# Kernel optimization log

Measured on AMD Instinct MI355X. Metric: run time of the kernel, lower is better.

Reference implementation:

```python
import jax, jax.numpy as jnp
import numpy as np

N, D, R, E = 20000, 256, 12, 200000  # nodes, feat dim, relation labels, edges


def setup_inputs() -> dict:
    key = jax.random.key(0)
    ks = jax.random.split(key, 8)
    x = jax.random.normal(ks[0], (N, D), dtype=jnp.float32)
    dep_idx = jax.random.randint(ks[1], (E,), 0, N)
    rel_idx = jax.random.randint(ks[2], (E,), 0, R)
    gov_idx = jax.random.randint(ks[3], (E,), 0, N)
    # nn.Linear params: W is [out,in], y = x @ W.T + b
    W_self = jax.random.normal(ks[4], (D, D), dtype=jnp.float32) * 0.02
    b_self = jnp.zeros((D,), dtype=jnp.float32)
    # 2R relation weights: [0..R) forward labels, [R..2R) reversed '_r' labels
    W_rel = jax.random.normal(ks[5], (2 * R, D, D), dtype=jnp.float32) * 0.02
    b_rel = jax.random.normal(ks[6], (2 * R, D), dtype=jnp.float32) * 0.02
    return {"x": x, "dep_idx": dep_idx, "rel_idx": rel_idx, "gov_idx": gov_idx,
            "W_self": W_self, "b_self": b_self, "W_rel": W_rel, "b_rel": b_rel}


def reference(x, dep_idx, rel_idx, gov_idx, W_self, b_self, W_rel, b_rel):
    R_ = W_rel.shape[0] // 2
    # self transform for every node
    out = x @ W_self.T + b_self  # [N, D]
    # all-relation transform, grouped GEMM instead of per-edge Linear calls
    T = jnp.einsum('nd,rod->nro', x, W_rel)  # [N, 2R, D]
    # forward edges: dependent += W[rel] @ x[governor] + b[rel]
    msg_f = T[gov_idx, rel_idx] + b_rel[rel_idx]          # [E, D]
    # reverse edges: governor += W[rel_r] @ x[dependent] + b[rel_r]
    msg_r = T[dep_idx, rel_idx + R_] + b_rel[rel_idx + R_]  # [E, D]
    out = out.at[dep_idx].add(msg_f).at[gov_idx].add(msg_r)
    return jax.nn.relu(out)
```

## Files before the change

kernel.cpp:

```cpp
#include <hip/hip_runtime.h>
#include <cstdint>
#include <cstddef>

#define DD 256
#define NSLOT 25
#define SELFSLOT 12

typedef unsigned short u16;
typedef __bf16 bf16t;
typedef bf16t bf16x8 __attribute__((ext_vector_type(8)));
typedef unsigned short us8 __attribute__((ext_vector_type(8)));
typedef unsigned short us4 __attribute__((ext_vector_type(4)));
typedef float f32x4 __attribute__((ext_vector_type(4)));

__device__ __forceinline__ u16 f2bf(float f) {
    uint32_t u = __builtin_bit_cast(uint32_t, f);
    u += 0x7FFFu + ((u >> 16) & 1u);
    return (u16)(u >> 16);
}
__device__ __forceinline__ float bf2f(u16 h) {
    uint32_t u = ((uint32_t)h) << 16;
    return __builtin_bit_cast(float, u);
}

__global__ void k_convert(const float* __restrict__ s, u16* __restrict__ d, int n) {
    int i = blockIdx.x * blockDim.x + threadIdx.x;
    int st = gridDim.x * blockDim.x;
    for (; i < n; i += st) d[i] = f2bf(s[i]);
}

__global__ void k_bias(const float* __restrict__ b_self, const float* __restrict__ b_rel,
                       float* __restrict__ dst) {
    int i = blockIdx.x * 256 + threadIdx.x;
    if (i >= NSLOT * DD) return;
    int s = i >> 8, n = i & 255;
    float v;
    if (s < SELFSLOT) v = b_rel[s * DD + n];
    else if (s == SELFSLOT) v = b_self[n];
    else v = b_rel[(s - 1) * DD + n];
    dst[i] = v;
}

__global__ void k_zero(int* p, int n) {
    int i = blockIdx.x * blockDim.x + threadIdx.x;
    if (i < n) p[i] = 0;
}

__global__ void k_mark(const int* __restrict__ dep, const int* __restrict__ rel,
                       const int* __restrict__ gov, int E, int N, int* __restrict__ flag) {
    int i = blockIdx.x * blockDim.x + threadIdx.x;
    int st = gridDim.x * blockDim.x;
    for (int j = i; j < E; j += st) {
        int r = rel[j];
        flag[r * N + gov[j]] = 1;
        flag[(13 + r) * N + dep[j]] = 1;
    }
    for (int j = i; j < N; j += st) flag[SELFSLOT * N + j] = 1;
}

__global__ void k_scan1(const int* __restrict__ counts, int* __restrict__ csr,
                        int* __restrict__ bsum, int B2) {
    __shared__ int sm[256];
    int tid = threadIdx.x;
    int i = blockIdx.x * 256 + tid;
    int v = (i < B2) ? counts[i] : 0;
    sm[tid] = v;
    __syncthreads();
    for (int off = 1; off < 256; off <<= 1) {
        int t = (tid >= off) ? sm[tid - off] : 0;
        __syncthreads();
        sm[tid] += t;
        __syncthreads();
    }
    if (i < B2) csr[i] = sm[tid] - v;
    if (tid == 255) bsum[blockIdx.x] = sm[255];
}

__global__ void k_scan2(const int* __restrict__ bsum, int* __restrict__ bbase, int nb) {
    __shared__ int sm[256];
    int t = threadIdx.x;
    int pre[8];
    int tot = 0;
    for (int j = 0; j < 8; ++j) {
        int idx = t * 8 + j;
        int v = (idx < nb) ? bsum[idx] : 0;
        pre[j] = tot;
        tot += v;
    }
    sm[t] = tot;
    __syncthreads();
    for (int off = 1; off < 256; off <<= 1) {
        int x = (t >= off) ? sm[t - off] : 0;
        __syncthreads();
        sm[t] += x;
        __syncthreads();
    }
    int base = sm[t] - tot;
    for (int j = 0; j < 8; ++j) {
        int idx = t * 8 + j;
        if (idx < nb) bbase[idx] = base + pre[j];
    }
}

__global__ void k_scan3f(int* __restrict__ pos, const int* __restrict__ bbase,
                         const int* __restrict__ flag, int B2) {
    int i = blockIdx.x * 256 + threadIdx.x;
    if (i < B2) {
        int v = pos[i] + bbase[i >> 8];
        pos[i] = v;
        if (i == B2 - 1) pos[B2] = v + flag[i];
    }
}

__global__ void k_scan3(int* __restrict__ csr, int* __restrict__ cursor,
                        const int* __restrict__ bbase, int B2, int E2) {
    int i = blockIdx.x * 256 + threadIdx.x;
    if (i < B2) {
        int v = csr[i] + bbase[i >> 8];
        csr[i] = v;
        cursor[i] = v;
    }
    if (i == 0) csr[B2] = E2;
}

__global__ void k_rk(const int* __restrict__ flag, const int* __restrict__ pos,
                     int* __restrict__ rksrc, int NN, int N) {
    int i = blockIdx.x * 256 + threadIdx.x;
    if (i >= NN) return;
    if (flag[i]) {
        int slot = i / N;
        rksrc[pos[i]] = i - slot * N;
    }
}

__global__ void k_hist(const int* __restrict__ dep, const int* __restrict__ rel,
                       const int* __restrict__ gov, int E, int N, int SG,
                       int* __restrict__ cnt) {
    int i = blockIdx.x * blockDim.x + threadIdx.x;
    int st = gridDim.x * blockDim.x;
    for (; i < E; i += st) {
        int r = rel[i];
        atomicAdd(&cnt[(r / SG) * N + dep[i]], 1);
        atomicAdd(&cnt[((13 + r) / SG) * N + gov[i]], 1);
    }
}

__global__ void k_scatter(const int* __restrict__ dep, const int* __restrict__ rel,
                          const int* __restrict__ gov, int E, int N, int SG,
                          const int* __restrict__ pos,
                          int* __restrict__ cursor, int* __restrict__ epay) {
    int i = blockIdx.x * blockDim.x + threadIdx.x;
    int st = gridDim.x * blockDim.x;
    for (; i < E; i += st) {
        int r = rel[i], d = dep[i], g = gov[i];
        int g0 = r / SG;
        int p = atomicAdd(&cursor[g0 * N + d], 1);
        epay[p] = pos[r * N + g] - pos[g0 * SG * N];
        int gs = 13 + r;
        int g1 = gs / SG;
        int q = atomicAdd(&cursor[g1 * N + g], 1);
        epay[q] = pos[gs * N + d] - pos[g1 * SG * N];
    }
}

__global__ __launch_bounds__(256) void k_T(
    const u16* __restrict__ xb, const u16* __restrict__ Wb, const float* __restrict__ ba,
    const int* __restrict__ pos, const int* __restrict__ rksrc, u16* __restrict__ T,
    int N, int gslot0, int tilesPerSlot) {
    __shared__ u16 sm[2 * 128 * 72];
    __shared__ int s_src[128];
    u16 (*As)[72] = (u16(*)[72])sm;
    u16 (*Bs)[72] = (u16(*)[72])(sm + 128 * 72);

    const int bx = blockIdx.x;
    const int slot = bx / tilesPerSlot;
    const int mtile = bx - slot * tilesPerSlot;
    const int gslot = gslot0 + slot;
    const int u0 = pos[gslot * N];
    const int used = pos[(gslot + 1) * N] - u0;
    const int row0 = mtile * 128;
    if (row0 >= used) return;
    const int gbase = pos[gslot0 * N];
    const int n0 = blockIdx.y * 128;
    const int tid = threadIdx.x;

    if (tid < 128) {
        int r = row0 + tid;
        s_src[tid] = rksrc[u0 + ((r < used) ? r : (used - 1))];
    }
    __syncthreads();

    const int lane = tid & 63, wv = tid >> 6;
    const int wr = wv & 1, wc = wv >> 1;
    const int l15 = lane & 15, quad = lane >> 4;
    const int srow = tid >> 1, sh = (tid & 1) * 32;
    const u16* bgp = Wb + ((size_t)gslot << 16) + (size_t)(n0 + srow) * DD + sh;

    f32x4 acc[4][4] = {};
    for (int kb = 0; kb < DD; kb += 64) {
        {
            const us8* ga = (const us8*)(xb + (size_t)s_src[srow] * DD + kb + sh);
            us8 a0 = ga[0], a1 = ga[1], a2 = ga[2], a3 = ga[3];
            *(us8*)&As[srow][sh]      = a0;
            *(us8*)&As[srow][sh + 8]  = a1;
            *(us8*)&As[srow][sh + 16] = a2;
            *(us8*)&As[srow][sh + 24] = a3;
            const us8* gb = (const us8*)(bgp + kb);
            us8 b0 = gb[0], b1 = gb[1], b2 = gb[2], b3 = gb[3];
            *(us8*)&Bs[srow][sh]      = b0;
            *(us8*)&Bs[srow][sh + 8]  = b1;
            *(us8*)&Bs[srow][sh + 16] = b2;
            *(us8*)&Bs[srow][sh + 24] = b3;
        }
        __syncthreads();
        #pragma unroll
        for (int ks = 0; ks < 2; ++ks) {
            const int kk = ks * 32 + quad * 8;
            bf16x8 af[4], bfv[4];
            #pragma unroll
            for (int mt = 0; mt < 4; ++mt)
                af[mt] = __builtin_bit_cast(bf16x8, *(const us8*)&As[wr * 64 + mt * 16 + l15][kk]);
            #pragma unroll
            for (int nt = 0; nt < 4; ++nt)
                bfv[nt] = __builtin_bit_cast(bf16x8, *(const us8*)&Bs[wc * 64 + nt * 16 + l15][kk]);
            #pragma unroll
            for (int mt = 0; mt < 4; ++mt)
                #pragma unroll
                for (int nt = 0; nt < 4; ++nt)
                    acc[mt][nt] = __builtin_amdgcn_mfma_f32_16x16x32_bf16(
                        af[mt], bfv[nt], acc[mt][nt], 0, 0, 0);
        }
        __syncthreads();
    }

    float bv[4];
    #pragma unroll
    for (int nt = 0; nt < 4; ++nt) bv[nt] = ba[gslot * DD + n0 + wc * 64 + nt * 16 + l15];
    u16* trb = sm + wv * (64 * 72);
    #pragma unroll
    for (int nt = 0; nt < 4; ++nt)
        #pragma unroll
        for (int mt = 0; mt < 4; ++mt)
            #pragma unroll
            for (int j = 0; j < 4; ++j)
                trb[(mt * 16 + quad * 4 + j) * 72 + nt * 16 + l15] =
                    f2bf(acc[mt][nt][j] + bv[nt]);
    __syncthreads();
    const int trow0 = u0 - gbase + row0 + wr * 64;
    const int half = lane & 1;
    #pragma unroll
    for (int it = 0; it < 2; ++it) {
        int r = it * 32 + (lane >> 1);
        if (row0 + wr * 64 + r < used) {
            const us8* sp = (const us8*)(trb + r * 72 + half * 32);
            us8 v0 = sp[0], v1 = sp[1], v2 = sp[2], v3 = sp[3];
            us8* dp = (us8*)(T + (size_t)(trow0 + r) * DD + n0 + wc * 64 + half * 32);
            dp[0] = v0; dp[1] = v1; dp[2] = v2; dp[3] = v3;
        }
    }
}

__global__ __launch_bounds__(256) void k_gather(
    const u16* __restrict__ T, const int* __restrict__ epay,
    const int* __restrict__ csr, const int* __restrict__ pos,
    float* __restrict__ out, int N, int bktBase, int selfKeyBase, int gfN,
    int first, int last) {
    int wid = (blockIdx.x * 256 + threadIdx.x) >> 6;
    if (wid >= N) return;
    int feat = (threadIdx.x & 63) * 4;
    f32x4 a = {0.0f, 0.0f, 0.0f, 0.0f};
    if (!first) a = *(const f32x4*)(out + (size_t)wid * DD + feat);
    if (selfKeyBase >= 0) {
        int p = pos[selfKeyBase + wid] - pos[gfN];
        us4 v = *(const us4*)(T + (size_t)p * DD + feat);
        a[0] += bf2f(v[0]); a[1] += bf2f(v[1]); a[2] += bf2f(v[2]); a[3] += bf2f(v[3]);
    }
    int beg = csr[bktBase + wid], end = csr[bktBase + wid + 1];
    f32x4 b = {0.0f, 0.0f, 0.0f, 0.0f};
    int j = beg;
    for (; j + 1 < end; j += 2) {
        int p0 = epay[j], p1 = epay[j + 1];
        us4 v0 = *(const us4*)(T + (size_t)p0 * DD + feat);
        us4 v1 = *(const us4*)(T + (size_t)p1 * DD + feat);
        a[0] += bf2f(v0[0]); a[1] += bf2f(v0[1]); a[2] += bf2f(v0[2]); a[3] += bf2f(v0[3]);
        b[0] += bf2f(v1[0]); b[1] += bf2f(v1[1]); b[2] += bf2f(v1[2]); b[3] += bf2f(v1[3]);
    }
    if (j < end) {
        int p0 = epay[j];
        us4 v0 = *(const us4*)(T + (size_t)p0 * DD + feat);
        a[0] += bf2f(v0[0]); a[1] += bf2f(v0[1]); a[2] += bf2f(v0[2]); a[3] += bf2f(v0[3]);
    }
    a[0] += b[0]; a[1] += b[1]; a[2] += b[2]; a[3] += b[3];
    if (last) {
        a[0] = fmaxf(a[0], 0.0f); a[1] = fmaxf(a[1], 0.0f);
        a[2] = fmaxf(a[2], 0.0f); a[3] = fmaxf(a[3], 0.0f);
    }
    *(f32x4*)(out + (size_t)wid * DD + feat) = a;
}

extern "C" void kernel_launch(void* const* d_in, const int* in_sizes, int n_in,
                              void* d_out, int out_size, void* d_ws, size_t ws_size,
                              hipStream_t stream) {
    const float* x      = (const float*)d_in[0];
    const int*   dep    = (const int*)  d_in[1];
    const int*   rel    = (const int*)  d_in[2];
    const int*   gov    = (const int*)  d_in[3];
    const float* W_self = (const float*)d_in[4];
    const float* b_self = (const float*)d_in[5];
    const float* W_rel  = (const float*)d_in[6];
    const float* b_rel  = (const float*)d_in[7];
    float* out = (float*)d_out;

    const int N  = in_sizes[0] / DD;
    const int E  = in_sizes[1];
    const int NN = NSLOT * N;

    char* w = (char*)d_ws;
    auto alloc = [&](size_t bytes) {
        char* p = w;
        w += (bytes + 255) & ~(size_t)255;
        return p;
    };
    u16* xb    = (u16*)alloc((size_t)N * DD * sizeof(u16));
    u16* Wb    = (u16*)alloc((size_t)NSLOT * DD * DD * sizeof(u16));
    float* ba  = (float*)alloc((size_t)NSLOT * DD * sizeof(float));
    int* flag  = (int*)alloc((size_t)NN * sizeof(int));
    int* pos   = (int*)alloc(((size_t)NN + 1) * sizeof(int));
    int* rksrc = (int*)alloc(((size_t)2 * E + N) * sizeof(int));
    int* bcsr  = (int*)alloc(((size_t)6 * N + 1) * sizeof(int));
    int* bcur  = (int*)alloc((size_t)6 * N * sizeof(int));
    int* bsum  = (int*)alloc((size_t)2048 * sizeof(int));
    int* bbas  = (int*)alloc((size_t)2048 * sizeof(int));
    int* epay  = (int*)alloc((size_t)2 * E * sizeof(int));

    size_t used = (size_t)(w - (char*)d_ws);
    size_t avail = (ws_size > used) ? (ws_size - used) : 0;

    int NGROUP = 2, SG = 13;
    for (int ng = 1; ng <= 5; ++ng) {
        int sg = (NSLOT + ng - 1) / ng;
        size_t maxB = 0;
        for (int g = 0; g < ng; ++g) {
            int s0 = g * sg, s1 = s0 + sg; if (s1 > NSLOT) s1 = NSLOT;
            if (s0 >= NSLOT) break;
            int hasSelf = (s0 <= SELFSLOT && SELFSLOT < s1) ? 1 : 0;
            size_t rels = (size_t)(s1 - s0 - hasSelf);
            size_t rows = rels * N; if (rows > (size_t)2 * E) rows = (size_t)2 * E;
            rows += hasSelf ? (size_t)N : 0;
            if (rows > maxB) maxB = rows;
        }
        if (maxB * ((size_t)DD * 2) <= avail) { NGROUP = ng; SG = sg; break; }
        NGROUP = ng + 1; SG = (NSLOT + NGROUP - 1) / NGROUP;
    }
    u16* T = (u16*)w;

    k_convert<<<1024, 256, 0, stream>>>(x, xb, N * DD);
    k_convert<<<1024, 256, 0, stream>>>(W_rel, Wb, 12 * DD * DD);
    k_convert<<<64, 256, 0, stream>>>(W_self, Wb + (size_t)SELFSLOT * DD * DD, DD * DD);
    k_convert<<<1024, 256, 0, stream>>>(W_rel + (size_t)12 * DD * DD,
                                        Wb + (size_t)13 * DD * DD, 12 * DD * DD);
    k_bias<<<(NSLOT * DD + 255) / 256, 256, 0, stream>>>(b_self, b_rel, ba);

    const int fBlocks = (NN + 255) / 256;
    k_zero<<<fBlocks, 256, 0, stream>>>(flag, NN);
    k_mark<<<512, 256, 0, stream>>>(dep, rel, gov, E, N, flag);
    k_scan1<<<fBlocks, 256, 0, stream>>>(flag, pos, bsum, NN);
    k_scan2<<<1, 256, 0, stream>>>(bsum, bbas, fBlocks);
    k_scan3f<<<fBlocks, 256, 0, stream>>>(pos, bbas, flag, NN);
    k_rk<<<fBlocks, 256, 0, stream>>>(flag, pos, rksrc, NN, N);

    int* bcnt = flag;
    const int B2 = NGROUP * N;
    const int bBlocks = (B2 + 255) / 256;
    k_zero<<<bBlocks, 256, 0, stream>>>(bcnt, B2);
    k_hist<<<256, 256, 0, stream>>>(dep, rel, gov, E, N, SG, bcnt);
    k_scan1<<<bBlocks, 256, 0, stream>>>(bcnt, bcsr, bsum, B2);
    k_scan2<<<1, 256, 0, stream>>>(bsum, bbas, bBlocks);
    k_scan3<<<bBlocks, 256, 0, stream>>>(bcsr, bcur, bbas, B2, 2 * E);
    k_scatter<<<(E + 255) / 256, 256, 0, stream>>>(dep, rel, gov, E, N, SG, pos, bcur, epay);

    const int tilesPerSlot = (N + 127) / 128;
    const int gBlocks = (N + 3) / 4;
    for (int g = 0; g < NGROUP; ++g) {
        int s0 = g * SG;
        if (s0 >= NSLOT) break;
        int Sg = NSLOT - s0; if (Sg > SG) Sg = SG;
        k_T<<<dim3(Sg * tilesPerSlot, 2), 256, 0, stream>>>(
            xb, Wb, ba, pos, rksrc, T, N, s0, tilesPerSlot);
        int hasSelf = (s0 <= SELFSLOT && SELFSLOT < s0 + Sg);
        k_gather<<<gBlocks, 256, 0, stream>>>(
            T, epay, bcsr, pos, out, N, g * N,
            hasSelf ? SELFSLOT * N : -1, s0 * N,
            (g == 0) ? 1 : 0, (g == NGROUP - 1) ? 1 : 0);
    }
}
```

Baseline: 305.8 us.

## Fuse preprocessing kernels and unroll gather loop by four

Merges the five conversion/bias kernels into one, fuses flag marking with the bucket histogram, and runs the two prefix-scan pipelines together in shared scan kernels. The rank-source build and the CSR finalisation are folded into one third-pass kernel, and zeroing switches to memset. The goal is to cut roughly a dozen small launches and their serialization gaps. The gather loop is also unrolled to four independent accumulators for more memory-level parallelism, and the histogram now gets its own buffer instead of reusing flag.

```diff
diff --git a/kernel.cpp b/kernel.cpp
--- a/kernel.cpp
+++ b/kernel.cpp
@@ -23,47 +23,64 @@
     return __builtin_bit_cast(float, u);
 }
 
-__global__ void k_convert(const float* __restrict__ s, u16* __restrict__ d, int n) {
+__global__ void k_convert_all(const float* __restrict__ x, const float* __restrict__ W_rel,
+                              const float* __restrict__ W_self, const float* __restrict__ b_self,
+                              const float* __restrict__ b_rel,
+                              u16* __restrict__ xb, u16* __restrict__ Wb,
+                              float* __restrict__ ba, int NDD) {
+    const int s0 = NDD;
+    const int s1 = s0 + 12 * 65536;
+    const int s2 = s1 + 65536;
+    const int s3 = s2 + 12 * 65536;
+    const int s4 = s3 + NSLOT * DD;
     int i = blockIdx.x * blockDim.x + threadIdx.x;
     int st = gridDim.x * blockDim.x;
-    for (; i < n; i += st) d[i] = f2bf(s[i]);
-}
-
-__global__ void k_bias(const float* __restrict__ b_self, const float* __restrict__ b_rel,
-                       float* __restrict__ dst) {
-    int i = blockIdx.x * 256 + threadIdx.x;
-    if (i >= NSLOT * DD) return;
-    int s = i >> 8, n = i & 255;
-    float v;
-    if (s < SELFSLOT) v = b_rel[s * DD + n];
-    else if (s == SELFSLOT) v = b_self[n];
-    else v = b_rel[(s - 1) * DD + n];
-    dst[i] = v;
-}
-
-__global__ void k_zero(int* p, int n) {
-    int i = blockIdx.x * blockDim.x + threadIdx.x;
-    if (i < n) p[i] = 0;
-}
-
-__global__ void k_mark(const int* __restrict__ dep, const int* __restrict__ rel,
-                       const int* __restrict__ gov, int E, int N, int* __restrict__ flag) {
+    for (; i < s4; i += st) {
+        if (i < s0) {
+            xb[i] = f2bf(x[i]);
+        } else if (i < s1) {
+            int k = i - s0; Wb[k] = f2bf(W_rel[k]);
+        } else if (i < s2) {
+            int k = i - s1; Wb[12 * 65536 + k] = f2bf(W_self[k]);
+        } else if (i < s3) {
+            int k = i - s2; Wb[13 * 65536 + k] = f2bf(W_rel[12 * 65536 + k]);
+        } else {
+            int k = i - s3;
+            float v;
+            if (k < 12 * DD) v = b_rel[k];
+            else if (k < 13 * DD) v = b_self[k - 12 * DD];
+            else v = b_rel[k - DD];
+            ba[k] = v;
+        }
+    }
+}
+
+__global__ void k_markhist(const int* __restrict__ dep, const int* __restrict__ rel,
+                           const int* __restrict__ gov, int E, int N, int SG,
+                           int* __restrict__ flag, int* __restrict__ bcnt) {
     int i = blockIdx.x * blockDim.x + threadIdx.x;
     int st = gridDim.x * blockDim.x;
     for (int j = i; j < E; j += st) {
-        int r = rel[j];
-        flag[r * N + gov[j]] = 1;
-        flag[(13 + r) * N + dep[j]] = 1;
+        int r = rel[j], d = dep[j], g = gov[j];
+        flag[r * N + g] = 1;
+        flag[(13 + r) * N + d] = 1;
+        atomicAdd(&bcnt[(r / SG) * N + d], 1);
+        atomicAdd(&bcnt[((13 + r) / SG) * N + g], 1);
     }
     for (int j = i; j < N; j += st) flag[SELFSLOT * N + j] = 1;
 }
 
-__global__ void k_scan1(const int* __restrict__ counts, int* __restrict__ csr,
-                        int* __restrict__ bsum, int B2) {
+__global__ void k_scan1d(const int* __restrict__ A, int* __restrict__ outA,
+                         int* __restrict__ bsumA, int lenA, int nbA,
+                         const int* __restrict__ B, int* __restrict__ outB,
+                         int* __restrict__ bsumB, int lenB) {
     __shared__ int sm[256];
+    const int* in; int* outp; int* bs; int len; int lb;
+    if ((int)blockIdx.x < nbA) { in = A; outp = outA; bs = bsumA; len = lenA; lb = blockIdx.x; }
+    else { in = B; outp = outB; bs = bsumB; len = lenB; lb = blockIdx.x - nbA; }
     int tid = threadIdx.x;
-    int i = blockIdx.x * 256 + tid;
-    int v = (i < B2) ? counts[i] : 0;
+    int i = lb * 256 + tid;
+    int v = (i < len) ? in[i] : 0;
     sm[tid] = v;
     __syncthreads();
     for (int off = 1; off < 256; off <<= 1) {
@@ -72,77 +89,64 @@
         sm[tid] += t;
         __syncthreads();
     }
-    if (i < B2) csr[i] = sm[tid] - v;
-    if (tid == 255) bsum[blockIdx.x] = sm[255];
-}
-
-__global__ void k_scan2(const int* __restrict__ bsum, int* __restrict__ bbase, int nb) {
+    if (i < len) outp[i] = sm[tid] - v;
+    if (tid == 255) bs[lb] = sm[255];
+}
+
+__global__ void k_scan2d(const int* __restrict__ bsumA, int* __restrict__ bbasA, int nbA,
+                         const int* __restrict__ bsumB, int* __restrict__ bbasB, int nbB) {
     __shared__ int sm[256];
     int t = threadIdx.x;
-    int pre[8];
-    int tot = 0;
-    for (int j = 0; j < 8; ++j) {
-        int idx = t * 8 + j;
-        int v = (idx < nb) ? bsum[idx] : 0;
-        pre[j] = tot;
-        tot += v;
-    }
-    sm[t] = tot;
-    __syncthreads();
-    for (int off = 1; off < 256; off <<= 1) {
-        int x = (t >= off) ? sm[t - off] : 0;
-        __syncthreads();
-        sm[t] += x;
-        __syncthreads();
-    }
-    int base = sm[t] - tot;
-    for (int j = 0; j < 8; ++j) {
-        int idx = t * 8 + j;
-        if (idx < nb) bbase[idx] = base + pre[j];
-    }
-}
-
-__global__ void k_scan3f(int* __restrict__ pos, const int* __restrict__ bbase,
-                         const int* __restrict__ flag, int B2) {
+    for (int which = 0; which < 2; ++which) {
+        const int* bsum = which ? bsumB : bsumA;
+        int* bbase = which ? bbasB : bbasA;
+        int nb = which ? nbB : nbA;
+        int pre[8];
+        int tot = 0;
+        for (int j = 0; j < 8; ++j) {
+            int idx = t * 8 + j;
+            int v = (idx < nb) ? bsum[idx] : 0;
+            pre[j] = tot;
+            tot += v;
+        }
+        sm[t] = tot;
+        __syncthreads();
+        for (int off = 1; off < 256; off <<= 1) {
+            int x = (t >= off) ? sm[t - off] : 0;
+            __syncthreads();
+            sm[t] += x;
+            __syncthreads();
+        }
+        int base = sm[t] - tot;
+        for (int j = 0; j < 8; ++j) {
+            int idx = t * 8 + j;
+            if (idx < nb) bbase[idx] = base + pre[j];
+        }
+        __syncthreads();
+    }
+}
+
+__global__ void k_scan3d(int* __restrict__ pos, const int* __restrict__ bbasA,
+                         const int* __restrict__ flag, int NN, int N,
+                         int* __restrict__ rksrc,
+                         int* __restrict__ bcsr, int* __restrict__ bcur,
+                         const int* __restrict__ bbasB, int B2, int E2) {
     int i = blockIdx.x * 256 + threadIdx.x;
+    if (i < NN) {
+        int v = pos[i] + bbasA[i >> 8];
+        pos[i] = v;
+        if (i == NN - 1) pos[NN] = v + flag[i];
+        if (flag[i]) {
+            int slot = i / N;
+            rksrc[v] = i - slot * N;
+        }
+    }
     if (i < B2) {
-        int v = pos[i] + bbase[i >> 8];
-        pos[i] = v;
-        if (i == B2 - 1) pos[B2] = v + flag[i];
-    }
-}
-
-__global__ void k_scan3(int* __restrict__ csr, int* __restrict__ cursor,
-                        const int* __restrict__ bbase, int B2, int E2) {
-    int i = blockIdx.x * 256 + threadIdx.x;
-    if (i < B2) {
-        int v = csr[i] + bbase[i >> 8];
-        csr[i] = v;
-        cursor[i] = v;
-    }
-    if (i == 0) csr[B2] = E2;
-}
-
-__global__ void k_rk(const int* __restrict__ flag, const int* __restrict__ pos,
-                     int* __restrict__ rksrc, int NN, int N) {
-    int i = blockIdx.x * 256 + threadIdx.x;
-    if (i >= NN) return;
-    if (flag[i]) {
-        int slot = i / N;
-        rksrc[pos[i]] = i - slot * N;
-    }
-}
-
-__global__ void k_hist(const int* __restrict__ dep, const int* __restrict__ rel,
-                       const int* __restrict__ gov, int E, int N, int SG,
-                       int* __restrict__ cnt) {
-    int i = blockIdx.x * blockDim.x + threadIdx.x;
-    int st = gridDim.x * blockDim.x;
-    for (; i < E; i += st) {
-        int r = rel[i];
-        atomicAdd(&cnt[(r / SG) * N + dep[i]], 1);
-        atomicAdd(&cnt[((13 + r) / SG) * N + gov[i]], 1);
-    }
+        int v = bcsr[i] + bbasB[i >> 8];
+        bcsr[i] = v;
+        bcur[i] = v;
+    }
+    if (i == 0) bcsr[B2] = E2;
 }
 
 __global__ void k_scatter(const int* __restrict__ dep, const int* __restrict__ rel,
@@ -276,21 +280,28 @@
         a[0] += bf2f(v[0]); a[1] += bf2f(v[1]); a[2] += bf2f(v[2]); a[3] += bf2f(v[3]);
     }
     int beg = csr[bktBase + wid], end = csr[bktBase + wid + 1];
-    f32x4 b = {0.0f, 0.0f, 0.0f, 0.0f};
+    f32x4 b = {0, 0, 0, 0}, c = {0, 0, 0, 0}, d4 = {0, 0, 0, 0};
     int j = beg;
-    for (; j + 1 < end; j += 2) {
-        int p0 = epay[j], p1 = epay[j + 1];
+    for (; j + 3 < end; j += 4) {
+        int p0 = epay[j], p1 = epay[j + 1], p2 = epay[j + 2], p3 = epay[j + 3];
         us4 v0 = *(const us4*)(T + (size_t)p0 * DD + feat);
         us4 v1 = *(const us4*)(T + (size_t)p1 * DD + feat);
+        us4 v2 = *(const us4*)(T + (size_t)p2 * DD + feat);
+        us4 v3 = *(const us4*)(T + (size_t)p3 * DD + feat);
         a[0] += bf2f(v0[0]); a[1] += bf2f(v0[1]); a[2] += bf2f(v0[2]); a[3] += bf2f(v0[3]);
         b[0] += bf2f(v1[0]); b[1] += bf2f(v1[1]); b[2] += bf2f(v1[2]); b[3] += bf2f(v1[3]);
-    }
-    if (j < end) {
+        c[0] += bf2f(v2[0]); c[1] += bf2f(v2[1]); c[2] += bf2f(v2[2]); c[3] += bf2f(v2[3]);
+        d4[0] += bf2f(v3[0]); d4[1] += bf2f(v3[1]); d4[2] += bf2f(v3[2]); d4[3] += bf2f(v3[3]);
+    }
+    for (; j < end; ++j) {
         int p0 = epay[j];
         us4 v0 = *(const us4*)(T + (size_t)p0 * DD + feat);
         a[0] += bf2f(v0[0]); a[1] += bf2f(v0[1]); a[2] += bf2f(v0[2]); a[3] += bf2f(v0[3]);
     }
-    a[0] += b[0]; a[1] += b[1]; a[2] += b[2]; a[3] += b[3];
+    a[0] += b[0] + c[0] + d4[0];
+    a[1] += b[1] + c[1] + d4[1];
+    a[2] += b[2] + c[2] + d4[2];
+    a[3] += b[3] + c[3] + d4[3];
     if (last) {
         a[0] = fmaxf(a[0], 0.0f); a[1] = fmaxf(a[1], 0.0f);
         a[2] = fmaxf(a[2], 0.0f); a[3] = fmaxf(a[3], 0.0f);
@@ -327,10 +338,13 @@
     int* flag  = (int*)alloc((size_t)NN * sizeof(int));
     int* pos   = (int*)alloc(((size_t)NN + 1) * sizeof(int));
     int* rksrc = (int*)alloc(((size_t)2 * E + N) * sizeof(int));
+    int* bcnt  = (int*)alloc((size_t)6 * N * sizeof(int));
     int* bcsr  = (int*)alloc(((size_t)6 * N + 1) * sizeof(int));
     int* bcur  = (int*)alloc((size_t)6 * N * sizeof(int));
-    int* bsum  = (int*)alloc((size_t)2048 * sizeof(int));
-    int* bbas  = (int*)alloc((size_t)2048 * sizeof(int));
+    int* bsumA = (int*)alloc((size_t)2048 * sizeof(int));
+    int* bbasA = (int*)alloc((size_t)2048 * sizeof(int));
+    int* bsumB = (int*)alloc((size_t)2048 * sizeof(int));
+    int* bbasB = (int*)alloc((size_t)2048 * sizeof(int));
     int* epay  = (int*)alloc((size_t)2 * E * sizeof(int));
 
     size_t used = (size_t)(w - (char*)d_ws);
@@ -353,30 +367,21 @@
         NGROUP = ng + 1; SG = (NSLOT + NGROUP - 1) / NGROUP;
     }
     u16* T = (u16*)w;
-
-    k_convert<<<1024, 256, 0, stream>>>(x, xb, N * DD);
-    k_convert<<<1024, 256, 0, stream>>>(W_rel, Wb, 12 * DD * DD);
-    k_convert<<<64, 256, 0, stream>>>(W_self, Wb + (size_t)SELFSLOT * DD * DD, DD * DD);
-    k_convert<<<1024, 256, 0, stream>>>(W_rel + (size_t)12 * DD * DD,
-                                        Wb + (size_t)13 * DD * DD, 12 * DD * DD);
-    k_bias<<<(NSLOT * DD + 255) / 256, 256, 0, stream>>>(b_self, b_rel, ba);
-
-    const int fBlocks = (NN + 255) / 256;
-    k_zero<<<fBlocks, 256, 0, stream>>>(flag, NN);
-    k_mark<<<512, 256, 0, stream>>>(dep, rel, gov, E, N, flag);
-    k_scan1<<<fBlocks, 256, 0, stream>>>(flag, pos, bsum, NN);
-    k_scan2<<<1, 256, 0, stream>>>(bsum, bbas, fBlocks);
-    k_scan3f<<<fBlocks, 256, 0, stream>>>(pos, bbas, flag, NN);
-    k_rk<<<fBlocks, 256, 0, stream>>>(flag, pos, rksrc, NN, N);
-
-    int* bcnt = flag;
     const int B2 = NGROUP * N;
-    const int bBlocks = (B2 + 255) / 256;
-    k_zero<<<bBlocks, 256, 0, stream>>>(bcnt, B2);
-    k_hist<<<256, 256, 0, stream>>>(dep, rel, gov, E, N, SG, bcnt);
-    k_scan1<<<bBlocks, 256, 0, stream>>>(bcnt, bcsr, bsum, B2);
-    k_scan2<<<1, 256, 0, stream>>>(bsum, bbas, bBlocks);
-    k_scan3<<<bBlocks, 256, 0, stream>>>(bcsr, bcur, bbas, B2, 2 * E);
+
+    k_convert_all<<<1024, 256, 0, stream>>>(x, W_rel, W_self, b_self, b_rel,
+                                            xb, Wb, ba, N * DD);
+
+    hipMemsetAsync(flag, 0, (size_t)NN * sizeof(int), stream);
+    hipMemsetAsync(bcnt, 0, (size_t)B2 * sizeof(int), stream);
+    k_markhist<<<512, 256, 0, stream>>>(dep, rel, gov, E, N, SG, flag, bcnt);
+
+    const int nbA = (NN + 255) / 256;
+    const int nbB = (B2 + 255) / 256;
+    k_scan1d<<<nbA + nbB, 256, 0, stream>>>(flag, pos, bsumA, NN, nbA, bcnt, bcsr, bsumB, B2);
+    k_scan2d<<<1, 256, 0, stream>>>(bsumA, bbasA, nbA, bsumB, bbasB, nbB);
+    k_scan3d<<<nbA, 256, 0, stream>>>(pos, bbasA, flag, NN, N, rksrc, bcsr, bcur, bbasB, B2, 2 * E);
+
     k_scatter<<<(E + 255) / 256, 256, 0, stream>>>(dep, rel, gov, E, N, SG, pos, bcur, epay);
 
     const int tilesPerSlot = (N + 127) / 128;
```

Measured after the change: 290.9 us. 1.05x faster.
